# Optimization experiments

Hardware: AMD Instinct MI355X
Metric: run time of the kernel (lower is better)

The kernel has to match this reference:

```python
import jax, jax.numpy as jnp
import numpy as np

N_HEADS = 16
HEAD_DIM = 64


def apply_rope(x, cos, sin):
    # x: [B, H, S, D]; cos/sin: [S, D//2]
    x_even = x[..., ::2]
    x_odd = x[..., 1::2]
    c = cos[None, None, :, :]
    s = sin[None, None, :, :]
    rot_even = x_even * c - x_odd * s
    rot_odd = x_even * s + x_odd * c
    return jnp.stack((rot_even, rot_odd), axis=-1).reshape(x.shape)


def setup_inputs() -> dict:
    key = jax.random.key(0)
    ks = jax.random.split(key, 7)
    B, S, D = 2, 2048, 1024
    x = jax.random.normal(ks[0], (B, S, D), dtype=jnp.float32)
    # realistic rope tables
    inv_freq = 1.0 / (10000.0 ** (np.arange(0, HEAD_DIM, 2, dtype=np.float32) / HEAD_DIM))
    t = np.arange(S, dtype=np.float32)
    freqs = np.outer(t, inv_freq)  # [S, HEAD_DIM//2]
    rope_cos = jnp.asarray(np.cos(freqs), dtype=jnp.float32)
    rope_sin = jnp.asarray(np.sin(freqs), dtype=jnp.float32)
    Wqkv = jax.random.normal(ks[1], (D, 3 * D), dtype=jnp.float32) * (D ** -0.5)
    bqkv = jax.random.normal(ks[2], (3 * D,), dtype=jnp.float32) * 0.02
    Wout = jax.random.normal(ks[3], (D, D), dtype=jnp.float32) * (D ** -0.5)
    bout = jax.random.normal(ks[4], (D,), dtype=jnp.float32) * 0.02
    return {"x": x, "rope_cos": rope_cos, "rope_sin": rope_sin,
            "Wqkv": Wqkv, "bqkv": bqkv, "Wout": Wout, "bout": bout}


def reference(x, rope_cos, rope_sin, Wqkv, bqkv, Wout, bout):
    B, S, D = x.shape
    H, Hd = N_HEADS, HEAD_DIM
    qkv = x @ Wqkv + bqkv                      # [B, S, 3D]
    qkv = qkv.reshape(B, S, 3, H, Hd).transpose(2, 0, 3, 1, 4)  # [3, B, H, S, Hd]
    q, k, v = qkv[0], qkv[1], qkv[2]
    q = apply_rope(q, rope_cos, rope_sin)
    k = apply_rope(k, rope_cos, rope_sin)
    scale = Hd ** -0.5
    scores = jnp.einsum('bhqd,bhkd->bhqk', q, k) * scale
    causal = jnp.tril(jnp.ones((S, S), dtype=bool))
    scores = jnp.where(causal[None, None], scores, jnp.finfo(scores.dtype).min)
    attn = jax.nn.softmax(scores, axis=-1)
    out = jnp.einsum('bhqk,bhkd->bhqd', attn, v)  # [B, H, S, Hd]
    out = out.transpose(0, 2, 1, 3).reshape(B, S, D)
    return out @ Wout + bout
```

## Files before the change

kernel.cpp:

```cpp
#include <hip/hip_runtime.h>
#include <hip/hip_bf16.h>

typedef unsigned short u16;
typedef __attribute__((ext_vector_type(4))) float f32x4;
typedef __attribute__((ext_vector_type(16))) float f32x16;
typedef __attribute__((ext_vector_type(8))) short short8;
typedef __attribute__((ext_vector_type(8))) unsigned short ushort8;

__device__ __forceinline__ u16 f2bf(float f) {
  union { float f; unsigned u; } v; v.f = f;
  unsigned r = v.u + 0x7fffu + ((v.u >> 16) & 1u);
  return (u16)(r >> 16);
}
__device__ __forceinline__ float b2f(u16 h) {
  union { unsigned u; float f; } v; v.u = ((unsigned)h) << 16;
  return v.f;
}
__device__ __forceinline__ f32x4 mfma16(short8 a, short8 b, f32x4 c) {
  return __builtin_amdgcn_mfma_f32_16x16x32_bf16(a, b, c, 0, 0, 0);
}
__device__ __forceinline__ f32x16 mfma32(short8 a, short8 b, f32x16 c) {
  return __builtin_amdgcn_mfma_f32_32x32x16_bf16(a, b, c, 0, 0, 0);
}
__device__ __forceinline__ unsigned cvtpk(float a, float b) {
  unsigned r;
  asm("v_cvt_pk_bf16_f32 %0, %1, %2" : "=v"(r) : "v"(a), "v"(b));
  return r;
}
__device__ __forceinline__ short8 pack4(unsigned w0, unsigned w1, unsigned w2, unsigned w3) {
  union { unsigned u[4]; short8 s; } t;
  t.u[0] = w0; t.u[1] = w1; t.u[2] = w2; t.u[3] = w3;
  return t.s;
}
__device__ __forceinline__ float exp2h(float x) { return __builtin_amdgcn_exp2f(x); }

__global__ __launch_bounds__(256) void cvt_f32_bf16_k(const float* __restrict__ in,
                                                      u16* __restrict__ out, int n8) {
  int t = blockIdx.x * 256 + threadIdx.x;
  if (t >= n8) return;
  const float4* p = (const float4*)(in + (size_t)t * 8);
  float4 a = p[0], b = p[1];
  ushort8 o;
  o[0] = f2bf(a.x); o[1] = f2bf(a.y); o[2] = f2bf(a.z); o[3] = f2bf(a.w);
  o[4] = f2bf(b.x); o[5] = f2bf(b.y); o[6] = f2bf(b.z); o[7] = f2bf(b.w);
  *(ushort8*)(out + (size_t)t * 8) = o;
}

__global__ __launch_bounds__(256) void transpose_f32_bf16_k(const float* __restrict__ in,
                                                            u16* __restrict__ out, int R, int C) {
  __shared__ float tile[32][33];
  int bc = blockIdx.x * 32, br = blockIdx.y * 32;
  int tx = threadIdx.x & 31, ty = threadIdx.x >> 5;
#pragma unroll
  for (int p = 0; p < 4; ++p)
    tile[ty + p * 8][tx] = in[(size_t)(br + ty + p * 8) * C + bc + tx];
  __syncthreads();
#pragma unroll
  for (int p = 0; p < 4; ++p)
    out[(size_t)(bc + ty + p * 8) * R + br + tx] = f2bf(tile[tx][ty + p * 8]);
}

template <int MODE>
__global__ __launch_bounds__(256) void gemm_bt_k(const u16* __restrict__ A,
                                                 const u16* __restrict__ Bt,
                                                 const float* __restrict__ bias,
                                                 const float* __restrict__ cosT,
                                                 const float* __restrict__ sinT,
                                                 void* __restrict__ Cout) {
  __shared__ __align__(16) u16 As[128 * 32];
  __shared__ __align__(16) u16 Bs[128 * 32];
  const int tid = threadIdx.x, lane = tid & 63, w = tid >> 6;
  const int wr = w >> 1, wc = w & 1, g = lane >> 4, c16 = lane & 15;
  const int rowBase = blockIdx.y * 128, colBase = blockIdx.x * 128;
  f32x4 acc[4][4] = {};
  const int e0 = (w * 2 + 0) * 512 + lane * 8;
  const int e1 = (w * 2 + 1) * 512 + lane * 8;
  const u16* Ag0 = A + (size_t)(rowBase + (e0 >> 5)) * 1024 + (e0 & 31);
  const u16* Ag1 = A + (size_t)(rowBase + (e1 >> 5)) * 1024 + (e1 & 31);
  const u16* Bg0 = Bt + (size_t)(colBase + (e0 >> 5)) * 1024 + (e0 & 31);
  const u16* Bg1 = Bt + (size_t)(colBase + (e1 >> 5)) * 1024 + (e1 & 31);
  u16* As0 = As + (w * 2 + 0) * 512;
  u16* As1 = As + (w * 2 + 1) * 512;
  u16* Bs0 = Bs + (w * 2 + 0) * 512;
  u16* Bs1 = Bs + (w * 2 + 1) * 512;
  for (int k0 = 0; k0 < 1024; k0 += 32) {
    __builtin_amdgcn_global_load_lds((const __attribute__((address_space(1))) void*)(Ag0 + k0),
                                     (__attribute__((address_space(3))) void*)As0, 16, 0, 0);
    __builtin_amdgcn_global_load_lds((const __attribute__((address_space(1))) void*)(Ag1 + k0),
                                     (__attribute__((address_space(3))) void*)As1, 16, 0, 0);
    __builtin_amdgcn_global_load_lds((const __attribute__((address_space(1))) void*)(Bg0 + k0),
                                     (__attribute__((address_space(3))) void*)Bs0, 16, 0, 0);
    __builtin_amdgcn_global_load_lds((const __attribute__((address_space(1))) void*)(Bg1 + k0),
                                     (__attribute__((address_space(3))) void*)Bs1, 16, 0, 0);
    asm volatile("s_waitcnt vmcnt(0)" ::: "memory");
    __syncthreads();
    short8 af[4], bfr[4];
#pragma unroll
    for (int t = 0; t < 4; ++t)
      af[t] = *(const short8*)(As + ((wr * 64 + t * 16 + c16) * 32 + g * 8));
#pragma unroll
    for (int t = 0; t < 4; ++t)
      bfr[t] = *(const short8*)(Bs + ((wc * 64 + t * 16 + c16) * 32 + g * 8));
#pragma unroll
    for (int i = 0; i < 4; ++i)
#pragma unroll
      for (int j = 0; j < 4; ++j) acc[i][j] = mfma16(af[i], bfr[j], acc[i][j]);
    __syncthreads();
  }
#pragma unroll
  for (int i = 0; i < 4; ++i) {
    int mbase = rowBase + wr * 64 + i * 16 + 4 * g;
#pragma unroll
    for (int j = 0; j < 4; ++j) {
      int n = colBase + wc * 64 + j * 16 + c16;
      float bv = bias[n];
#pragma unroll
      for (int r = 0; r < 4; ++r) {
        float v = acc[i][j][r] + bv;
        int m = mbase + r;
        if (MODE == 0) {
          int which = n >> 10, hh = (n >> 6) & 15, d = n & 63;
          int bb = m >> 11, s = m & 2047;
          float outv = v;
          if (which < 2) {
            float pv = __shfl_xor(v, 1);
            float cc = cosT[(size_t)s * 32 + (d >> 1)];
            float ss = sinT[(size_t)s * 32 + (d >> 1)];
            outv = (d & 1) ? (v * cc + pv * ss) : (v * cc - pv * ss);
            if (which == 0) outv *= 0.18033688f;
          }
          ((u16*)Cout)[((size_t)(((which * 2 + bb) * 16 + hh) * 2048 + s) << 6) + d] = f2bf(outv);
        } else {
          ((float*)Cout)[(size_t)m * 1024 + n] = v;
        }
      }
    }
  }
}

__global__ __launch_bounds__(256) void vtrans_k(const u16* __restrict__ V, u16* __restrict__ Vt) {
  __shared__ u16 t[64][72];
  const int bh = blockIdx.y, s0 = blockIdx.x * 64;
  const u16* src = V + ((size_t)bh << 17);
  u16* dst = Vt + ((size_t)bh << 17);
  const int r = threadIdx.x >> 2, c0 = (threadIdx.x & 3) * 16;
  *(short8*)&t[r][c0] = *(const short8*)(src + (size_t)(s0 + r) * 64 + c0);
  *(short8*)&t[r][c0 + 8] = *(const short8*)(src + (size_t)(s0 + r) * 64 + c0 + 8);
  __syncthreads();
  const int d = threadIdx.x >> 2, sc0 = (threadIdx.x & 3) * 16;
  ushort8 o0, o1;
#pragma unroll
  for (int e = 0; e < 8; ++e) { o0[e] = t[sc0 + e][d]; o1[e] = t[sc0 + 8 + e][d]; }
  *(ushort8*)(dst + (size_t)d * 2048 + s0 + sc0) = o0;
  *(ushort8*)(dst + (size_t)d * 2048 + s0 + sc0 + 8) = o1;
}

__global__ __launch_bounds__(256, 2) void attn7_k(const u16* __restrict__ Qm,
                                                  const u16* __restrict__ Km,
                                                  const u16* __restrict__ Vtm,
                                                  u16* __restrict__ Om) {
  __shared__ __align__(16) u16 KL[2][4096];
  __shared__ __align__(16) u16 VL[2][4096];

  const int tid = threadIdx.x;
  const int lane = tid & 63, w = tid >> 6;
  const int x = blockIdx.x & 7;
  const int i = blockIdx.x >> 3;
  const int bh = 4 * x + (i & 3);
  const int rank = i >> 2;
  const int qm = (rank < 8) ? (15 - rank) : (rank - 8);
  const int b = bh >> 4, hd = bh & 15;
  const int qb = qm * 128 + w * 32;
  const int q32 = lane & 31, hl = lane >> 5;
  const int nt = 2 * qm + 2;

  const u16* Qp = Qm + ((size_t)bh << 17);
  const u16* Kp = Km + ((size_t)bh << 17);
  const u16* Vtp = Vtm + ((size_t)bh << 17);

  const u16* qrow = Qp + ((size_t)(qb + q32) << 6) + 8 * hl;
  short8 qf[4];
#pragma unroll
  for (int ks = 0; ks < 4; ++ks) qf[ks] = *(const short8*)(qrow + 16 * ks);

  f32x16 acc0 = {}, acc1 = {};
  float m_run = -1e30f, l_run = 0.f;
  const int qg = qb + q32;
  const int rr = w * 8 + (lane >> 3);
  const int sb = (lane & 7) ^ (lane >> 3);
  const int swz = q32 & 7;

  auto stage = [&](int buf, int k0s) {
    u16* kb = &KL[buf][w * 512];
    u16* vb = &VL[buf][w * 512];
    __builtin_amdgcn_global_load_lds(
        (const __attribute__((address_space(1))) void*)(Kp + ((size_t)(k0s + rr) << 6) + sb * 8),
        (__attribute__((address_space(3))) void*)kb, 16, 0, 0);
    __builtin_amdgcn_global_load_lds(
        (const __attribute__((address_space(1))) void*)(Kp + ((size_t)(k0s + rr + 32) << 6) + sb * 8),
        (__attribute__((address_space(3))) void*)(kb + 2048), 16, 0, 0);
    __builtin_amdgcn_global_load_lds(
        (const __attribute__((address_space(1))) void*)(Vtp + ((size_t)rr << 11) + k0s + sb * 8),
        (__attribute__((address_space(3))) void*)vb, 16, 0, 0);
    __builtin_amdgcn_global_load_lds(
        (const __attribute__((address_space(1))) void*)(Vtp + ((size_t)(rr + 32) << 11) + k0s + sb * 8),
        (__attribute__((address_space(3))) void*)(vb + 2048), 16, 0, 0);
  };

  stage(0, 0);
  asm volatile("s_waitcnt vmcnt(0)" ::: "memory");
  __syncthreads();

  for (int it = 0; it < nt; ++it) {
    const int cur = it & 1;
    if (it + 1 < nt) stage(cur ^ 1, 64 * (it + 1));
    const int k0 = 64 * it;

    if (k0 <= qb + 31) {
      const u16* Kb = &KL[cur][0];
      const u16* Vb = &VL[cur][0];

      f32x16 s0 = {}, s1 = {};
      __builtin_amdgcn_s_setprio(1);
#pragma unroll
      for (int ks = 0; ks < 4; ++ks) {
        const int cb = ((2 * ks + hl) ^ swz) * 8;
        short8 kf0 = *(const short8*)(Kb + q32 * 64 + cb);
        short8 kf1 = *(const short8*)(Kb + (32 + q32) * 64 + cb);
        s0 = mfma32(kf0, qf[ks], s0);
        s1 = mfma32(kf1, qf[ks], s1);
      }
      __builtin_amdgcn_s_setprio(0);

      short8 vfa[4], vfb[4];
#pragma unroll
      for (int ks = 0; ks < 4; ++ks) {
        const int cb = ((2 * ks + hl) ^ swz) * 8;
        vfa[ks] = *(const short8*)(Vb + q32 * 64 + cb);
        vfb[ks] = *(const short8*)(Vb + (32 + q32) * 64 + cb);
      }

      if (k0 + 63 > qb) {
#pragma unroll
        for (int r = 0; r < 16; ++r) {
          const int kvl = k0 + (r & 3) + 8 * (r >> 2) + 4 * hl;
          s0[r] = (kvl <= qg) ? s0[r] : -1e30f;
          s1[r] = (kvl + 32 <= qg) ? s1[r] : -1e30f;
        }
      }

      float pmax = s0[0];
#pragma unroll
      for (int r = 1; r < 16; ++r) pmax = fmaxf(pmax, s0[r]);
#pragma unroll
      for (int r = 0; r < 16; ++r) pmax = fmaxf(pmax, s1[r]);
      pmax = fmaxf(pmax, __shfl_xor(pmax, 32));

      if (!__all(pmax <= m_run + 11.5f)) {
        const float mn = fmaxf(m_run, pmax);
        const float alpha = exp2h(m_run - mn);
        l_run *= alpha;
        m_run = mn;
#pragma unroll
        for (int r = 0; r < 16; ++r) {
          const int row = (r & 3) + 8 * (r >> 2) + 4 * hl;
          const float ar = __shfl(alpha, row);
          acc0[r] *= ar; acc1[r] *= ar;
        }
      }

      float rs = 0.f;
#pragma unroll
      for (int r = 0; r < 16; ++r) { s0[r] = exp2h(s0[r] - m_run); rs += s0[r]; }
#pragma unroll
      for (int r = 0; r < 16; ++r) { s1[r] = exp2h(s1[r] - m_run); rs += s1[r]; }
      rs += __shfl_xor(rs, 32);
      l_run += rs;

      short8 pa[4];
#pragma unroll
      for (int t = 0; t < 2; ++t) {
        float p0, p1, p2, p3, p4, p5, p6, p7, p8, p9, pa_, pb_, pc_, pd_, pe_, pf_;
        if (t == 0) {
          p0 = s0[0];  p1 = s0[1];  p2 = s0[2];  p3 = s0[3];
          p4 = s0[4];  p5 = s0[5];  p6 = s0[6];  p7 = s0[7];
          p8 = s0[8];  p9 = s0[9];  pa_ = s0[10]; pb_ = s0[11];
          pc_ = s0[12]; pd_ = s0[13]; pe_ = s0[14]; pf_ = s0[15];
        } else {
          p0 = s1[0];  p1 = s1[1];  p2 = s1[2];  p3 = s1[3];
          p4 = s1[4];  p5 = s1[5];  p6 = s1[6];  p7 = s1[7];
          p8 = s1[8];  p9 = s1[9];  pa_ = s1[10]; pb_ = s1[11];
          pc_ = s1[12]; pd_ = s1[13]; pe_ = s1[14]; pf_ = s1[15];
        }
        const unsigned a0 = cvtpk(p0, p1), a1 = cvtpk(p2, p3);
        const unsigned a2 = cvtpk(p4, p5), a3 = cvtpk(p6, p7);
        const unsigned b0 = cvtpk(p8, p9), b1 = cvtpk(pa_, pb_);
        const unsigned b2 = cvtpk(pc_, pd_), b3 = cvtpk(pe_, pf_);
        const unsigned r0 = __shfl_xor(hl ? a0 : a2, 32);
        const unsigned r1 = __shfl_xor(hl ? a1 : a3, 32);
        pa[2 * t] = hl ? pack4(r0, r1, a2, a3) : pack4(a0, a1, r0, r1);
        const unsigned r2 = __shfl_xor(hl ? b0 : b2, 32);
        const unsigned r3 = __shfl_xor(hl ? b1 : b3, 32);
        pa[2 * t + 1] = hl ? pack4(r2, r3, b2, b3) : pack4(b0, b1, r2, r3);
      }

      __builtin_amdgcn_s_setprio(1);
#pragma unroll
      for (int ks = 0; ks < 4; ++ks) {
        acc0 = mfma32(pa[ks], vfa[ks], acc0);
        acc1 = mfma32(pa[ks], vfb[ks], acc1);
      }
      __builtin_amdgcn_s_setprio(0);
    }

    asm volatile("s_waitcnt vmcnt(0)" ::: "memory");
    __syncthreads();
  }

#pragma unroll
  for (int r = 0; r < 16; ++r) {
    const int row = (r & 3) + 8 * (r >> 2) + 4 * hl;
    const float li = 1.0f / __shfl(l_run, row);
    const int q = qb + row;
    const size_t base = ((size_t)(b * 2048 + q) << 10) + hd * 64 + q32;
    Om[base] = f2bf(acc0[r] * li);
    Om[base + 32] = f2bf(acc1[r] * li);
  }
}

extern "C" void kernel_launch(void* const* d_in, const int* in_sizes, int n_in,
                              void* d_out, int out_size, void* d_ws, size_t ws_size,
                              hipStream_t stream) {
  const float* x        = (const float*)d_in[0];
  const float* rope_cos = (const float*)d_in[1];
  const float* rope_sin = (const float*)d_in[2];
  const float* Wqkv     = (const float*)d_in[3];
  const float* bqkv     = (const float*)d_in[4];
  const float* Wout     = (const float*)d_in[5];
  const float* bout     = (const float*)d_in[6];
  float* out = (float*)d_out;
  char* ws = (char*)d_ws;

  u16* Xb      = (u16*)(ws);
  u16* WqkvT   = (u16*)(ws + 8388608);
  u16* WoutT   = (u16*)(ws + 14680064);
  u16* QKV     = (u16*)(ws + 16777216);
  u16* AttnOut = (u16*)(ws + 41943040);
  u16* Vt      = (u16*)(ws + 50331648);

  cvt_f32_bf16_k<<<dim3(2048), dim3(256), 0, stream>>>(x, Xb, 524288);
  transpose_f32_bf16_k<<<dim3(96, 32), dim3(256), 0, stream>>>(Wqkv, WqkvT, 1024, 3072);
  transpose_f32_bf16_k<<<dim3(32, 32), dim3(256), 0, stream>>>(Wout, WoutT, 1024, 1024);

  gemm_bt_k<0><<<dim3(24, 32), dim3(256), 0, stream>>>(Xb, WqkvT, bqkv, rope_cos, rope_sin,
                                                       (void*)QKV);

  u16* Qw = QKV;
  u16* Kw = QKV + (size_t)4194304;
  u16* Vw = QKV + (size_t)8388608;
  vtrans_k<<<dim3(32, 32), dim3(256), 0, stream>>>(Vw, Vt);
  attn7_k<<<dim3(512), dim3(256), 0, stream>>>(Qw, Kw, Vt, AttnOut);

  gemm_bt_k<1><<<dim3(8, 32), dim3(256), 0, stream>>>(AttnOut, WoutT, bout, nullptr, nullptr, out);
}
```

Measured before the change: 138.2 us.

## Replace QKV projection GEMM with 256x256-tiled, double-buffered, swizzled-LDS kernel

The QKV projection moves from 128x128 tiles with a 32-wide K step and a full wait every iteration to a new 512-thread kernel. It uses 256x256 tiles, a 64-wide K step, double-buffered LDS staging and an XOR-swizzled LDS layout, and interleaves global-to-LDS prefetch with MFMA quarters using sched barriers and setprio. The aim is more data reuse per tile, overlap of memory loads with compute, and fewer LDS bank conflicts in the largest GEMM. In exchange it needs 128 KB of LDS per block and many accumulator registers. With only 192 blocks it may underfill the 256 CUs. The output GEMM is split into its own plain kernel with no functional change.

New measurement: 150.1 us. 1.09x slower.

```diff
diff --git a/kernel.cpp b/kernel.cpp
--- a/kernel.cpp
+++ b/kernel.cpp
@@ -7,6 +7,9 @@
 typedef __attribute__((ext_vector_type(8))) short short8;
 typedef __attribute__((ext_vector_type(8))) unsigned short ushort8;
 
+#define AS1 __attribute__((address_space(1)))
+#define AS3 __attribute__((address_space(3)))
+
 __device__ __forceinline__ u16 f2bf(float f) {
   union { float f; unsigned u; } v; v.f = f;
   unsigned r = v.u + 0x7fffu + ((v.u >> 16) & 1u);
@@ -33,6 +36,9 @@
   return t.s;
 }
 __device__ __forceinline__ float exp2h(float x) { return __builtin_amdgcn_exp2f(x); }
+
+#define SBAR() do { __builtin_amdgcn_sched_barrier(0); __builtin_amdgcn_s_barrier(); \
+                    __builtin_amdgcn_sched_barrier(0); } while (0)
 
 __global__ __launch_bounds__(256) void cvt_f32_bf16_k(const float* __restrict__ in,
                                                       u16* __restrict__ out, int n8) {
@@ -60,13 +66,126 @@
     out[(size_t)(bc + ty + p * 8) * R + br + tx] = f2bf(tile[tx][ty + p * 8]);
 }
 
-template <int MODE>
-__global__ __launch_bounds__(256) void gemm_bt_k(const u16* __restrict__ A,
-                                                 const u16* __restrict__ Bt,
-                                                 const float* __restrict__ bias,
-                                                 const float* __restrict__ cosT,
-                                                 const float* __restrict__ sinT,
-                                                 void* __restrict__ Cout) {
+__global__ __launch_bounds__(512, 2) void gemm8_k(const u16* __restrict__ A,
+                                                  const u16* __restrict__ Bt,
+                                                  const float* __restrict__ bias,
+                                                  const float* __restrict__ cosT,
+                                                  const float* __restrict__ sinT,
+                                                  u16* __restrict__ Cout) {
+  __shared__ __align__(16) u16 As[2][16384];
+  __shared__ __align__(16) u16 Bs[2][16384];
+
+  const int tid = threadIdx.x, lane = tid & 63, w = tid >> 6;
+  const int wm = w >> 2, wn = w & 3;
+  const int g = lane >> 4, c16 = lane & 15;
+  const int l8 = lane >> 3, l7 = lane & 7;
+  const int bm = (blockIdx.x & 15) << 8;
+  const int bn = (blockIdx.x >> 4) << 8;
+
+  const int sw = (l7 ^ l8) * 8;
+  const int bs2 = (wn & 1) * 2 + wm;
+  const u16* Asrc = A + (size_t)(bm + wm * 128 + wn * 32 + l8) * 1024 + sw;
+  const u16* Bsrc = Bt + (size_t)(bn + (wn >> 1) * 128 + bs2 * 32 + l8) * 1024 + sw;
+  const int adst = wm * 8192 + wn * 2048;
+  const int bdst = (wn >> 1) * 8192 + bs2 * 2048;
+
+  f32x4 acc[8][4] = {};
+  short8 afr[8], bfr[8];
+  const int swr = (c16 & 7);
+
+#define STAGE_A(buf, kt) do { _Pragma("unroll") for (int j = 0; j < 4; ++j) \
+    __builtin_amdgcn_global_load_lds((const AS1 void*)(Asrc + (size_t)j * 8192 + (kt) * 64), \
+                                     (AS3 void*)(&As[buf][adst + j * 512]), 16, 0, 0); } while (0)
+#define STAGE_B(buf, kt) do { _Pragma("unroll") for (int j = 0; j < 4; ++j) \
+    __builtin_amdgcn_global_load_lds((const AS1 void*)(Bsrc + (size_t)j * 8192 + (kt) * 64), \
+                                     (AS3 void*)(&Bs[buf][bdst + j * 512]), 16, 0, 0); } while (0)
+#define LD_A(cur, MB) do { _Pragma("unroll") for (int mi = 0; mi < 4; ++mi) \
+    _Pragma("unroll") for (int kc = 0; kc < 2; ++kc) \
+      afr[mi * 2 + kc] = *(const short8*)(&As[cur][wm * 8192 + (((MB) + mi) * 16 + c16) * 64 + \
+                                                   (((kc * 4 + g) ^ swr) * 8)]); } while (0)
+#define LD_B(cur, NB, OFS) do { _Pragma("unroll") for (int nj = 0; nj < 2; ++nj) \
+    _Pragma("unroll") for (int kc = 0; kc < 2; ++kc) \
+      bfr[(OFS) + nj * 2 + kc] = *(const short8*)(&Bs[cur][(wn >> 1) * 8192 + \
+          ((wn & 1) * 64 + ((NB) + nj) * 16 + c16) * 64 + (((kc * 4 + g) ^ swr) * 8)]); } while (0)
+#define MFMA_Q(MB, NB, BOFS) do { _Pragma("unroll") for (int mi = 0; mi < 4; ++mi) \
+    _Pragma("unroll") for (int nj = 0; nj < 2; ++nj) \
+    _Pragma("unroll") for (int kc = 0; kc < 2; ++kc) \
+      acc[(MB) + mi][(NB) + nj] = mfma16(afr[mi * 2 + kc], bfr[(BOFS) + nj * 2 + kc], \
+                                         acc[(MB) + mi][(NB) + nj]); } while (0)
+
+  STAGE_A(0, 0);
+  STAGE_B(0, 0);
+  asm volatile("s_waitcnt vmcnt(0)" ::: "memory");
+  SBAR();
+
+  for (int t = 0; t < 16; ++t) {
+    const int cur = t & 1;
+    const bool pre = (t + 1 < 16);
+    LD_A(cur, 0);
+    LD_B(cur, 0, 0);
+    if (pre) STAGE_A(cur ^ 1, t + 1);
+    SBAR();
+    __builtin_amdgcn_s_setprio(1);
+    MFMA_Q(0, 0, 0);
+    __builtin_amdgcn_s_setprio(0);
+    SBAR();
+    LD_B(cur, 2, 4);
+    if (pre) STAGE_B(cur ^ 1, t + 1);
+    SBAR();
+    __builtin_amdgcn_s_setprio(1);
+    MFMA_Q(0, 2, 4);
+    __builtin_amdgcn_s_setprio(0);
+    SBAR();
+    LD_A(cur, 4);
+    SBAR();
+    __builtin_amdgcn_s_setprio(1);
+    MFMA_Q(4, 0, 0);
+    __builtin_amdgcn_s_setprio(0);
+    SBAR();
+    if (pre) { asm volatile("s_waitcnt vmcnt(0)" ::: "memory"); }
+    SBAR();
+    __builtin_amdgcn_s_setprio(1);
+    MFMA_Q(4, 2, 4);
+    __builtin_amdgcn_s_setprio(0);
+    SBAR();
+  }
+
+#pragma unroll
+  for (int mi = 0; mi < 8; ++mi) {
+    const int mbase = bm + wm * 128 + mi * 16 + 4 * g;
+#pragma unroll
+    for (int nj = 0; nj < 4; ++nj) {
+      const int n = bn + wn * 64 + nj * 16 + c16;
+      const float bv = bias[n];
+      const int which = n >> 10, hh = (n >> 6) & 15, d = n & 63;
+#pragma unroll
+      for (int r = 0; r < 4; ++r) {
+        float v = acc[mi][nj][r] + bv;
+        const int m = mbase + r;
+        const int bb = m >> 11, s = m & 2047;
+        float outv = v;
+        if (which < 2) {
+          float pv = __shfl_xor(v, 1);
+          float cc = cosT[(size_t)s * 32 + (d >> 1)];
+          float ssn = sinT[(size_t)s * 32 + (d >> 1)];
+          outv = (d & 1) ? (v * cc + pv * ssn) : (v * cc - pv * ssn);
+          if (which == 0) outv *= 0.18033688f;
+        }
+        Cout[((size_t)(((which * 2 + bb) * 16 + hh) * 2048 + s) << 6) + d] = f2bf(outv);
+      }
+    }
+  }
+#undef STAGE_A
+#undef STAGE_B
+#undef LD_A
+#undef LD_B
+#undef MFMA_Q
+}
+
+__global__ __launch_bounds__(256) void gemm_out_k(const u16* __restrict__ A,
+                                                  const u16* __restrict__ Bt,
+                                                  const float* __restrict__ bias,
+                                                  float* __restrict__ Cout) {
   __shared__ __align__(16) u16 As[128 * 32];
   __shared__ __align__(16) u16 Bs[128 * 32];
   const int tid = threadIdx.x, lane = tid & 63, w = tid >> 6;
@@ -84,27 +203,23 @@
   u16* Bs0 = Bs + (w * 2 + 0) * 512;
   u16* Bs1 = Bs + (w * 2 + 1) * 512;
   for (int k0 = 0; k0 < 1024; k0 += 32) {
-    __builtin_amdgcn_global_load_lds((const __attribute__((address_space(1))) void*)(Ag0 + k0),
-                                     (__attribute__((address_space(3))) void*)As0, 16, 0, 0);
-    __builtin_amdgcn_global_load_lds((const __attribute__((address_space(1))) void*)(Ag1 + k0),
-                                     (__attribute__((address_space(3))) void*)As1, 16, 0, 0);
-    __builtin_amdgcn_global_load_lds((const __attribute__((address_space(1))) void*)(Bg0 + k0),
-                                     (__attribute__((address_space(3))) void*)Bs0, 16, 0, 0);
-    __builtin_amdgcn_global_load_lds((const __attribute__((address_space(1))) void*)(Bg1 + k0),
-                                     (__attribute__((address_space(3))) void*)Bs1, 16, 0, 0);
+    __builtin_amdgcn_global_load_lds((const AS1 void*)(Ag0 + k0), (AS3 void*)As0, 16, 0, 0);
+    __builtin_amdgcn_global_load_lds((const AS1 void*)(Ag1 + k0), (AS3 void*)As1, 16, 0, 0);
+    __builtin_amdgcn_global_load_lds((const AS1 void*)(Bg0 + k0), (AS3 void*)Bs0, 16, 0, 0);
+    __builtin_amdgcn_global_load_lds((const AS1 void*)(Bg1 + k0), (AS3 void*)Bs1, 16, 0, 0);
     asm volatile("s_waitcnt vmcnt(0)" ::: "memory");
     __syncthreads();
-    short8 af[4], bfr[4];
+    short8 af[4], bfr2[4];
 #pragma unroll
     for (int t = 0; t < 4; ++t)
       af[t] = *(const short8*)(As + ((wr * 64 + t * 16 + c16) * 32 + g * 8));
 #pragma unroll
     for (int t = 0; t < 4; ++t)
-      bfr[t] = *(const short8*)(Bs + ((wc * 64 + t * 16 + c16) * 32 + g * 8));
+      bfr2[t] = *(const short8*)(Bs + ((wc * 64 + t * 16 + c16) * 32 + g * 8));
 #pragma unroll
     for (int i = 0; i < 4; ++i)
 #pragma unroll
-      for (int j = 0; j < 4; ++j) acc[i][j] = mfma16(af[i], bfr[j], acc[i][j]);
+      for (int j = 0; j < 4; ++j) acc[i][j] = mfma16(af[i], bfr2[j], acc[i][j]);
     __syncthreads();
   }
 #pragma unroll
@@ -115,25 +230,8 @@
       int n = colBase + wc * 64 + j * 16 + c16;
       float bv = bias[n];
 #pragma unroll
-      for (int r = 0; r < 4; ++r) {
-        float v = acc[i][j][r] + bv;
-        int m = mbase + r;
-        if (MODE == 0) {
-          int which = n >> 10, hh = (n >> 6) & 15, d = n & 63;
-          int bb = m >> 11, s = m & 2047;
-          float outv = v;
-          if (which < 2) {
-            float pv = __shfl_xor(v, 1);
-            float cc = cosT[(size_t)s * 32 + (d >> 1)];
-            float ss = sinT[(size_t)s * 32 + (d >> 1)];
-            outv = (d & 1) ? (v * cc + pv * ss) : (v * cc - pv * ss);
-            if (which == 0) outv *= 0.18033688f;
-          }
-          ((u16*)Cout)[((size_t)(((which * 2 + bb) * 16 + hh) * 2048 + s) << 6) + d] = f2bf(outv);
-        } else {
-          ((float*)Cout)[(size_t)m * 1024 + n] = v;
-        }
-      }
+      for (int r = 0; r < 4; ++r)
+        Cout[(size_t)(mbase + r) * 1024 + n] = acc[i][j][r] + bv;
     }
   }
 }
@@ -194,17 +292,17 @@
     u16* kb = &KL[buf][w * 512];
     u16* vb = &VL[buf][w * 512];
     __builtin_amdgcn_global_load_lds(
-        (const __attribute__((address_space(1))) void*)(Kp + ((size_t)(k0s + rr) << 6) + sb * 8),
-        (__attribute__((address_space(3))) void*)kb, 16, 0, 0);
+        (const AS1 void*)(Kp + ((size_t)(k0s + rr) << 6) + sb * 8),
+        (AS3 void*)kb, 16, 0, 0);
     __builtin_amdgcn_global_load_lds(
-        (const __attribute__((address_space(1))) void*)(Kp + ((size_t)(k0s + rr + 32) << 6) + sb * 8),
-        (__attribute__((address_space(3))) void*)(kb + 2048), 16, 0, 0);
+        (const AS1 void*)(Kp + ((size_t)(k0s + rr + 32) << 6) + sb * 8),
+        (AS3 void*)(kb + 2048), 16, 0, 0);
     __builtin_amdgcn_global_load_lds(
-        (const __attribute__((address_space(1))) void*)(Vtp + ((size_t)rr << 11) + k0s + sb * 8),
-        (__attribute__((address_space(3))) void*)vb, 16, 0, 0);
+        (const AS1 void*)(Vtp + ((size_t)rr << 11) + k0s + sb * 8),
+        (AS3 void*)vb, 16, 0, 0);
     __builtin_amdgcn_global_load_lds(
-        (const __attribute__((address_space(1))) void*)(Vtp + ((size_t)(rr + 32) << 11) + k0s + sb * 8),
-        (__attribute__((address_space(3))) void*)(vb + 2048), 16, 0, 0);
+        (const AS1 void*)(Vtp + ((size_t)(rr + 32) << 11) + k0s + sb * 8),
+        (AS3 void*)(vb + 2048), 16, 0, 0);
   };
 
   stage(0, 0);
@@ -352,8 +450,7 @@
   transpose_f32_bf16_k<<<dim3(96, 32), dim3(256), 0, stream>>>(Wqkv, WqkvT, 1024, 3072);
   transpose_f32_bf16_k<<<dim3(32, 32), dim3(256), 0, stream>>>(Wout, WoutT, 1024, 1024);
 
-  gemm_bt_k<0><<<dim3(24, 32), dim3(256), 0, stream>>>(Xb, WqkvT, bqkv, rope_cos, rope_sin,
-                                                       (void*)QKV);
+  gemm8_k<<<dim3(192), dim3(512), 0, stream>>>(Xb, WqkvT, bqkv, rope_cos, rope_sin, QKV);
 
   u16* Qw = QKV;
   u16* Kw = QKV + (size_t)4194304;
@@ -361,5 +458,5 @@
   vtrans_k<<<dim3(32, 32), dim3(256), 0, stream>>>(Vw, Vt);
   attn7_k<<<dim3(512), dim3(256), 0, stream>>>(Qw, Kw, Vt, AttnOut);
 
-  gemm_bt_k<1><<<dim3(8, 32), dim3(256), 0, stream>>>(AttnOut, WoutT, bout, nullptr, nullptr, out);
-}
+  gemm_out_k<<<dim3(8, 32), dim3(256), 0, stream>>>(AttnOut, WoutT, bout, out);
+}
```

## Split attention into 64-query blocks of two waves with snake-order scheduling

Applied to the files above, without the earlier changes.

The attention kernel now uses 128-thread blocks, each covering 64 query rows, and launches twice as many blocks. The causal tile count per block becomes qm+1, so no fully-masked KV tile is ever visited, and the per-tile skip branch is removed. Query blocks are assigned in a serpentine order within groups of eight to balance work across the grid. In exchange, each K/V tile staged into LDS is shared by only two waves instead of four, so global-to-LDS traffic per unit of compute goes up.

Result: slower. 145.0 us (+4.9%).

```diff
diff --git a/kernel.cpp b/kernel.cpp
--- a/kernel.cpp
+++ b/kernel.cpp
@@ -6,6 +6,9 @@
 typedef __attribute__((ext_vector_type(16))) float f32x16;
 typedef __attribute__((ext_vector_type(8))) short short8;
 typedef __attribute__((ext_vector_type(8))) unsigned short ushort8;
+
+#define AS1 __attribute__((address_space(1)))
+#define AS3 __attribute__((address_space(3)))
 
 __device__ __forceinline__ u16 f2bf(float f) {
   union { float f; unsigned u; } v; v.f = f;
@@ -84,14 +87,10 @@
   u16* Bs0 = Bs + (w * 2 + 0) * 512;
   u16* Bs1 = Bs + (w * 2 + 1) * 512;
   for (int k0 = 0; k0 < 1024; k0 += 32) {
-    __builtin_amdgcn_global_load_lds((const __attribute__((address_space(1))) void*)(Ag0 + k0),
-                                     (__attribute__((address_space(3))) void*)As0, 16, 0, 0);
-    __builtin_amdgcn_global_load_lds((const __attribute__((address_space(1))) void*)(Ag1 + k0),
-                                     (__attribute__((address_space(3))) void*)As1, 16, 0, 0);
-    __builtin_amdgcn_global_load_lds((const __attribute__((address_space(1))) void*)(Bg0 + k0),
-                                     (__attribute__((address_space(3))) void*)Bs0, 16, 0, 0);
-    __builtin_amdgcn_global_load_lds((const __attribute__((address_space(1))) void*)(Bg1 + k0),
-                                     (__attribute__((address_space(3))) void*)Bs1, 16, 0, 0);
+    __builtin_amdgcn_global_load_lds((const AS1 void*)(Ag0 + k0), (AS3 void*)As0, 16, 0, 0);
+    __builtin_amdgcn_global_load_lds((const AS1 void*)(Ag1 + k0), (AS3 void*)As1, 16, 0, 0);
+    __builtin_amdgcn_global_load_lds((const AS1 void*)(Bg0 + k0), (AS3 void*)Bs0, 16, 0, 0);
+    __builtin_amdgcn_global_load_lds((const AS1 void*)(Bg1 + k0), (AS3 void*)Bs1, 16, 0, 0);
     asm volatile("s_waitcnt vmcnt(0)" ::: "memory");
     __syncthreads();
     short8 af[4], bfr[4];
@@ -155,7 +154,7 @@
   *(ushort8*)(dst + (size_t)d * 2048 + s0 + sc0 + 8) = o1;
 }
 
-__global__ __launch_bounds__(256, 2) void attn7_k(const u16* __restrict__ Qm,
+__global__ __launch_bounds__(128, 4) void attn8_k(const u16* __restrict__ Qm,
                                                   const u16* __restrict__ Km,
                                                   const u16* __restrict__ Vtm,
                                                   u16* __restrict__ Om) {
@@ -168,11 +167,12 @@
   const int i = blockIdx.x >> 3;
   const int bh = 4 * x + (i & 3);
   const int rank = i >> 2;
-  const int qm = (rank < 8) ? (15 - rank) : (rank - 8);
+  const int sl = rank >> 3, g8 = rank & 7;
+  const int qm = (sl & 1) ? (8 * sl + 7 - g8) : (8 * sl + g8);
   const int b = bh >> 4, hd = bh & 15;
-  const int qb = qm * 128 + w * 32;
+  const int qb = qm * 64 + w * 32;
   const int q32 = lane & 31, hl = lane >> 5;
-  const int nt = 2 * qm + 2;
+  const int nt = qm + 1;
 
   const u16* Qp = Qm + ((size_t)bh << 17);
   const u16* Kp = Km + ((size_t)bh << 17);
@@ -186,25 +186,23 @@
   f32x16 acc0 = {}, acc1 = {};
   float m_run = -1e30f, l_run = 0.f;
   const int qg = qb + q32;
-  const int rr = w * 8 + (lane >> 3);
-  const int sb = (lane & 7) ^ (lane >> 3);
+  const int r8 = lane >> 3;
+  const int sb = (lane & 7) ^ r8;
   const int swz = q32 & 7;
 
   auto stage = [&](int buf, int k0s) {
-    u16* kb = &KL[buf][w * 512];
-    u16* vb = &VL[buf][w * 512];
-    __builtin_amdgcn_global_load_lds(
-        (const __attribute__((address_space(1))) void*)(Kp + ((size_t)(k0s + rr) << 6) + sb * 8),
-        (__attribute__((address_space(3))) void*)kb, 16, 0, 0);
-    __builtin_amdgcn_global_load_lds(
-        (const __attribute__((address_space(1))) void*)(Kp + ((size_t)(k0s + rr + 32) << 6) + sb * 8),
-        (__attribute__((address_space(3))) void*)(kb + 2048), 16, 0, 0);
-    __builtin_amdgcn_global_load_lds(
-        (const __attribute__((address_space(1))) void*)(Vtp + ((size_t)rr << 11) + k0s + sb * 8),
-        (__attribute__((address_space(3))) void*)vb, 16, 0, 0);
-    __builtin_amdgcn_global_load_lds(
-        (const __attribute__((address_space(1))) void*)(Vtp + ((size_t)(rr + 32) << 11) + k0s + sb * 8),
-        (__attribute__((address_space(3))) void*)(vb + 2048), 16, 0, 0);
+#pragma unroll
+    for (int j = 0; j < 4; ++j) {
+      const int row = j * 16 + w * 8 + r8;
+      const u16* ksrc = Kp + ((size_t)(k0s + row) << 6) + sb * 8;
+      __builtin_amdgcn_global_load_lds(
+          (const AS1 void*)ksrc,
+          (AS3 void*)(&KL[buf][(j * 16 + w * 8) * 64]), 16, 0, 0);
+      const u16* vsrc = Vtp + ((size_t)row << 11) + k0s + sb * 8;
+      __builtin_amdgcn_global_load_lds(
+          (const AS1 void*)vsrc,
+          (AS3 void*)(&VL[buf][(j * 16 + w * 8) * 64]), 16, 0, 0);
+    }
   };
 
   stage(0, 0);
@@ -216,102 +214,100 @@
     if (it + 1 < nt) stage(cur ^ 1, 64 * (it + 1));
     const int k0 = 64 * it;
 
-    if (k0 <= qb + 31) {
-      const u16* Kb = &KL[cur][0];
-      const u16* Vb = &VL[cur][0];
-
-      f32x16 s0 = {}, s1 = {};
-      __builtin_amdgcn_s_setprio(1);
-#pragma unroll
-      for (int ks = 0; ks < 4; ++ks) {
-        const int cb = ((2 * ks + hl) ^ swz) * 8;
-        short8 kf0 = *(const short8*)(Kb + q32 * 64 + cb);
-        short8 kf1 = *(const short8*)(Kb + (32 + q32) * 64 + cb);
-        s0 = mfma32(kf0, qf[ks], s0);
-        s1 = mfma32(kf1, qf[ks], s1);
+    const u16* Kb = &KL[cur][0];
+    const u16* Vb = &VL[cur][0];
+
+    f32x16 s0 = {}, s1 = {};
+    __builtin_amdgcn_s_setprio(1);
+#pragma unroll
+    for (int ks = 0; ks < 4; ++ks) {
+      const int cb = ((2 * ks + hl) ^ swz) * 8;
+      short8 kf0 = *(const short8*)(Kb + q32 * 64 + cb);
+      short8 kf1 = *(const short8*)(Kb + (32 + q32) * 64 + cb);
+      s0 = mfma32(kf0, qf[ks], s0);
+      s1 = mfma32(kf1, qf[ks], s1);
+    }
+    __builtin_amdgcn_s_setprio(0);
+
+    short8 vfa[4], vfb[4];
+#pragma unroll
+    for (int ks = 0; ks < 4; ++ks) {
+      const int cb = ((2 * ks + hl) ^ swz) * 8;
+      vfa[ks] = *(const short8*)(Vb + q32 * 64 + cb);
+      vfb[ks] = *(const short8*)(Vb + (32 + q32) * 64 + cb);
+    }
+
+    if (k0 + 63 > qb) {
+#pragma unroll
+      for (int r = 0; r < 16; ++r) {
+        const int kvl = k0 + (r & 3) + 8 * (r >> 2) + 4 * hl;
+        s0[r] = (kvl <= qg) ? s0[r] : -1e30f;
+        s1[r] = (kvl + 32 <= qg) ? s1[r] : -1e30f;
       }
-      __builtin_amdgcn_s_setprio(0);
-
-      short8 vfa[4], vfb[4];
-#pragma unroll
-      for (int ks = 0; ks < 4; ++ks) {
-        const int cb = ((2 * ks + hl) ^ swz) * 8;
-        vfa[ks] = *(const short8*)(Vb + q32 * 64 + cb);
-        vfb[ks] = *(const short8*)(Vb + (32 + q32) * 64 + cb);
+    }
+
+    float pmax = s0[0];
+#pragma unroll
+    for (int r = 1; r < 16; ++r) pmax = fmaxf(pmax, s0[r]);
+#pragma unroll
+    for (int r = 0; r < 16; ++r) pmax = fmaxf(pmax, s1[r]);
+    pmax = fmaxf(pmax, __shfl_xor(pmax, 32));
+
+    if (!__all(pmax <= m_run + 11.5f)) {
+      const float mn = fmaxf(m_run, pmax);
+      const float alpha = exp2h(m_run - mn);
+      l_run *= alpha;
+      m_run = mn;
+#pragma unroll
+      for (int r = 0; r < 16; ++r) {
+        const int row = (r & 3) + 8 * (r >> 2) + 4 * hl;
+        const float ar = __shfl(alpha, row);
+        acc0[r] *= ar; acc1[r] *= ar;
       }
-
-      if (k0 + 63 > qb) {
-#pragma unroll
-        for (int r = 0; r < 16; ++r) {
-          const int kvl = k0 + (r & 3) + 8 * (r >> 2) + 4 * hl;
-          s0[r] = (kvl <= qg) ? s0[r] : -1e30f;
-          s1[r] = (kvl + 32 <= qg) ? s1[r] : -1e30f;
-        }
+    }
+
+    float rs = 0.f;
+#pragma unroll
+    for (int r = 0; r < 16; ++r) { s0[r] = exp2h(s0[r] - m_run); rs += s0[r]; }
+#pragma unroll
+    for (int r = 0; r < 16; ++r) { s1[r] = exp2h(s1[r] - m_run); rs += s1[r]; }
+    rs += __shfl_xor(rs, 32);
+    l_run += rs;
+
+    short8 pa[4];
+#pragma unroll
+    for (int t = 0; t < 2; ++t) {
+      float p0, p1, p2, p3, p4, p5, p6, p7, p8, p9, pa_, pb_, pc_, pd_, pe_, pf_;
+      if (t == 0) {
+        p0 = s0[0];  p1 = s0[1];  p2 = s0[2];  p3 = s0[3];
+        p4 = s0[4];  p5 = s0[5];  p6 = s0[6];  p7 = s0[7];
+        p8 = s0[8];  p9 = s0[9];  pa_ = s0[10]; pb_ = s0[11];
+        pc_ = s0[12]; pd_ = s0[13]; pe_ = s0[14]; pf_ = s0[15];
+      } else {
+        p0 = s1[0];  p1 = s1[1];  p2 = s1[2];  p3 = s1[3];
+        p4 = s1[4];  p5 = s1[5];  p6 = s1[6];  p7 = s1[7];
+        p8 = s1[8];  p9 = s1[9];  pa_ = s1[10]; pb_ = s1[11];
+        pc_ = s1[12]; pd_ = s1[13]; pe_ = s1[14]; pf_ = s1[15];
       }
-
-      float pmax = s0[0];
-#pragma unroll
-      for (int r = 1; r < 16; ++r) pmax = fmaxf(pmax, s0[r]);
-#pragma unroll
-      for (int r = 0; r < 16; ++r) pmax = fmaxf(pmax, s1[r]);
-      pmax = fmaxf(pmax, __shfl_xor(pmax, 32));
-
-      if (!__all(pmax <= m_run + 11.5f)) {
-        const float mn = fmaxf(m_run, pmax);
-        const float alpha = exp2h(m_run - mn);
-        l_run *= alpha;
-        m_run = mn;
-#pragma unroll
-        for (int r = 0; r < 16; ++r) {
-          const int row = (r & 3) + 8 * (r >> 2) + 4 * hl;
-          const float ar = __shfl(alpha, row);
-          acc0[r] *= ar; acc1[r] *= ar;
-        }
-      }
-
-      float rs = 0.f;
-#pragma unroll
-      for (int r = 0; r < 16; ++r) { s0[r] = exp2h(s0[r] - m_run); rs += s0[r]; }
-#pragma unroll
-      for (int r = 0; r < 16; ++r) { s1[r] = exp2h(s1[r] - m_run); rs += s1[r]; }
-      rs += __shfl_xor(rs, 32);
-      l_run += rs;
-
-      short8 pa[4];
-#pragma unroll
-      for (int t = 0; t < 2; ++t) {
-        float p0, p1, p2, p3, p4, p5, p6, p7, p8, p9, pa_, pb_, pc_, pd_, pe_, pf_;
-        if (t == 0) {
-          p0 = s0[0];  p1 = s0[1];  p2 = s0[2];  p3 = s0[3];
-          p4 = s0[4];  p5 = s0[5];  p6 = s0[6];  p7 = s0[7];
-          p8 = s0[8];  p9 = s0[9];  pa_ = s0[10]; pb_ = s0[11];
-          pc_ = s0[12]; pd_ = s0[13]; pe_ = s0[14]; pf_ = s0[15];
-        } else {
-          p0 = s1[0];  p1 = s1[1];  p2 = s1[2];  p3 = s1[3];
-          p4 = s1[4];  p5 = s1[5];  p6 = s1[6];  p7 = s1[7];
-          p8 = s1[8];  p9 = s1[9];  pa_ = s1[10]; pb_ = s1[11];
-          pc_ = s1[12]; pd_ = s1[13]; pe_ = s1[14]; pf_ = s1[15];
-        }
-        const unsigned a0 = cvtpk(p0, p1), a1 = cvtpk(p2, p3);
-        const unsigned a2 = cvtpk(p4, p5), a3 = cvtpk(p6, p7);
-        const unsigned b0 = cvtpk(p8, p9), b1 = cvtpk(pa_, pb_);
-        const unsigned b2 = cvtpk(pc_, pd_), b3 = cvtpk(pe_, pf_);
-        const unsigned r0 = __shfl_xor(hl ? a0 : a2, 32);
-        const unsigned r1 = __shfl_xor(hl ? a1 : a3, 32);
-        pa[2 * t] = hl ? pack4(r0, r1, a2, a3) : pack4(a0, a1, r0, r1);
-        const unsigned r2 = __shfl_xor(hl ? b0 : b2, 32);
-        const unsigned r3 = __shfl_xor(hl ? b1 : b3, 32);
-        pa[2 * t + 1] = hl ? pack4(r2, r3, b2, b3) : pack4(b0, b1, r2, r3);
-      }
-
-      __builtin_amdgcn_s_setprio(1);
-#pragma unroll
-      for (int ks = 0; ks < 4; ++ks) {
-        acc0 = mfma32(pa[ks], vfa[ks], acc0);
-        acc1 = mfma32(pa[ks], vfb[ks], acc1);
-      }
-      __builtin_amdgcn_s_setprio(0);
-    }
+      const unsigned a0 = cvtpk(p0, p1), a1 = cvtpk(p2, p3);
+      const unsigned a2 = cvtpk(p4, p5), a3 = cvtpk(p6, p7);
+      const unsigned b0 = cvtpk(p8, p9), b1 = cvtpk(pa_, pb_);
+      const unsigned b2 = cvtpk(pc_, pd_), b3 = cvtpk(pe_, pf_);
+      const unsigned r0 = __shfl_xor(hl ? a0 : a2, 32);
+      const unsigned r1 = __shfl_xor(hl ? a1 : a3, 32);
+      pa[2 * t] = hl ? pack4(r0, r1, a2, a3) : pack4(a0, a1, r0, r1);
+      const unsigned r2 = __shfl_xor(hl ? b0 : b2, 32);
+      const unsigned r3 = __shfl_xor(hl ? b1 : b3, 32);
+      pa[2 * t + 1] = hl ? pack4(r2, r3, b2, b3) : pack4(b0, b1, r2, r3);
+    }
+
+    __builtin_amdgcn_s_setprio(1);
+#pragma unroll
+    for (int ks = 0; ks < 4; ++ks) {
+      acc0 = mfma32(pa[ks], vfa[ks], acc0);
+      acc1 = mfma32(pa[ks], vfb[ks], acc1);
+    }
+    __builtin_amdgcn_s_setprio(0);
 
     asm volatile("s_waitcnt vmcnt(0)" ::: "memory");
     __syncthreads();
@@ -359,7 +355,7 @@
   u16* Kw = QKV + (size_t)4194304;
   u16* Vw = QKV + (size_t)8388608;
   vtrans_k<<<dim3(32, 32), dim3(256), 0, stream>>>(Vw, Vt);
-  attn7_k<<<dim3(512), dim3(256), 0, stream>>>(Qw, Kw, Vt, AttnOut);
+  attn8_k<<<dim3(1024), dim3(128), 0, stream>>>(Qw, Kw, Vt, AttnOut);
 
   gemm_bt_k<1><<<dim3(8, 32), dim3(256), 0, stream>>>(AttnOut, WoutT, bout, nullptr, nullptr, out);
 }
```

## Double GEMM K-tile to 64 with XOR-swizzled LDS layout

Applied to the files above, without the earlier changes.

The projection GEMM now stages a 64-wide K slice per iteration instead of 32, halving the number of barrier/wait rounds over K. The LDS tile rows are 64 elements with an XOR swizzle on 16-byte chunks, applied on the global-load side and matched on the fragment reads, to avoid bank conflicts. LDS use doubles and each wave issues twice the MMAs per sync. The attention kernel is only touched cosmetically with address-space macros.

After: 156.3 us. 13.1% more time.

```diff
diff --git a/kernel.cpp b/kernel.cpp
--- a/kernel.cpp
+++ b/kernel.cpp
@@ -6,6 +6,9 @@
 typedef __attribute__((ext_vector_type(16))) float f32x16;
 typedef __attribute__((ext_vector_type(8))) short short8;
 typedef __attribute__((ext_vector_type(8))) unsigned short ushort8;
+
+#define AS1 __attribute__((address_space(1)))
+#define AS3 __attribute__((address_space(3)))
 
 __device__ __forceinline__ u16 f2bf(float f) {
   union { float f; unsigned u; } v; v.f = f;
@@ -67,46 +70,55 @@
                                                  const float* __restrict__ cosT,
                                                  const float* __restrict__ sinT,
                                                  void* __restrict__ Cout) {
-  __shared__ __align__(16) u16 As[128 * 32];
-  __shared__ __align__(16) u16 Bs[128 * 32];
+  __shared__ __align__(16) u16 As[128 * 64];
+  __shared__ __align__(16) u16 Bs[128 * 64];
   const int tid = threadIdx.x, lane = tid & 63, w = tid >> 6;
   const int wr = w >> 1, wc = w & 1, g = lane >> 4, c16 = lane & 15;
   const int rowBase = blockIdx.y * 128, colBase = blockIdx.x * 128;
+  const int r8 = lane >> 3, l7 = lane & 7;
+  const int sb = l7 ^ r8;
   f32x4 acc[4][4] = {};
-  const int e0 = (w * 2 + 0) * 512 + lane * 8;
-  const int e1 = (w * 2 + 1) * 512 + lane * 8;
-  const u16* Ag0 = A + (size_t)(rowBase + (e0 >> 5)) * 1024 + (e0 & 31);
-  const u16* Ag1 = A + (size_t)(rowBase + (e1 >> 5)) * 1024 + (e1 & 31);
-  const u16* Bg0 = Bt + (size_t)(colBase + (e0 >> 5)) * 1024 + (e0 & 31);
-  const u16* Bg1 = Bt + (size_t)(colBase + (e1 >> 5)) * 1024 + (e1 & 31);
-  u16* As0 = As + (w * 2 + 0) * 512;
-  u16* As1 = As + (w * 2 + 1) * 512;
-  u16* Bs0 = Bs + (w * 2 + 0) * 512;
-  u16* Bs1 = Bs + (w * 2 + 1) * 512;
-  for (int k0 = 0; k0 < 1024; k0 += 32) {
-    __builtin_amdgcn_global_load_lds((const __attribute__((address_space(1))) void*)(Ag0 + k0),
-                                     (__attribute__((address_space(3))) void*)As0, 16, 0, 0);
-    __builtin_amdgcn_global_load_lds((const __attribute__((address_space(1))) void*)(Ag1 + k0),
-                                     (__attribute__((address_space(3))) void*)As1, 16, 0, 0);
-    __builtin_amdgcn_global_load_lds((const __attribute__((address_space(1))) void*)(Bg0 + k0),
-                                     (__attribute__((address_space(3))) void*)Bs0, 16, 0, 0);
-    __builtin_amdgcn_global_load_lds((const __attribute__((address_space(1))) void*)(Bg1 + k0),
-                                     (__attribute__((address_space(3))) void*)Bs1, 16, 0, 0);
+
+  const u16* Ag[4];
+  const u16* Bg[4];
+#pragma unroll
+  for (int j = 0; j < 4; ++j) {
+    const int row = w * 32 + j * 8 + r8;
+    Ag[j] = A + (size_t)(rowBase + row) * 1024 + sb * 8;
+    Bg[j] = Bt + (size_t)(colBase + row) * 1024 + sb * 8;
+  }
+
+  for (int k0 = 0; k0 < 1024; k0 += 64) {
+#pragma unroll
+    for (int j = 0; j < 4; ++j) {
+      __builtin_amdgcn_global_load_lds((const AS1 void*)(Ag[j] + k0),
+                                       (AS3 void*)(As + (w * 2048 + j * 512)), 16, 0, 0);
+      __builtin_amdgcn_global_load_lds((const AS1 void*)(Bg[j] + k0),
+                                       (AS3 void*)(Bs + (w * 2048 + j * 512)), 16, 0, 0);
+    }
     asm volatile("s_waitcnt vmcnt(0)" ::: "memory");
     __syncthreads();
-    short8 af[4], bfr[4];
+    const int swr = c16 & 7;
+    short8 af[4][2], bfr[4][2];
 #pragma unroll
     for (int t = 0; t < 4; ++t)
-      af[t] = *(const short8*)(As + ((wr * 64 + t * 16 + c16) * 32 + g * 8));
-#pragma unroll
-    for (int t = 0; t < 4; ++t)
-      bfr[t] = *(const short8*)(Bs + ((wc * 64 + t * 16 + c16) * 32 + g * 8));
+#pragma unroll
+      for (int kc = 0; kc < 2; ++kc) {
+        af[t][kc] = *(const short8*)(As + (wr * 64 + t * 16 + c16) * 64 +
+                                     (((kc * 4 + g) ^ swr) * 8));
+        bfr[t][kc] = *(const short8*)(Bs + (wc * 64 + t * 16 + c16) * 64 +
+                                      (((kc * 4 + g) ^ swr) * 8));
+      }
 #pragma unroll
     for (int i = 0; i < 4; ++i)
 #pragma unroll
-      for (int j = 0; j < 4; ++j) acc[i][j] = mfma16(af[i], bfr[j], acc[i][j]);
+      for (int j = 0; j < 4; ++j) {
+        acc[i][j] = mfma16(af[i][0], bfr[j][0], acc[i][j]);
+        acc[i][j] = mfma16(af[i][1], bfr[j][1], acc[i][j]);
+      }
     __syncthreads();
   }
+
 #pragma unroll
   for (int i = 0; i < 4; ++i) {
     int mbase = rowBase + wr * 64 + i * 16 + 4 * g;
@@ -194,17 +206,17 @@
     u16* kb = &KL[buf][w * 512];
     u16* vb = &VL[buf][w * 512];
     __builtin_amdgcn_global_load_lds(
-        (const __attribute__((address_space(1))) void*)(Kp + ((size_t)(k0s + rr) << 6) + sb * 8),
-        (__attribute__((address_space(3))) void*)kb, 16, 0, 0);
+        (const AS1 void*)(Kp + ((size_t)(k0s + rr) << 6) + sb * 8),
+        (AS3 void*)kb, 16, 0, 0);
     __builtin_amdgcn_global_load_lds(
-        (const __attribute__((address_space(1))) void*)(Kp + ((size_t)(k0s + rr + 32) << 6) + sb * 8),
-        (__attribute__((address_space(3))) void*)(kb + 2048), 16, 0, 0);
+        (const AS1 void*)(Kp + ((size_t)(k0s + rr + 32) << 6) + sb * 8),
+        (AS3 void*)(kb + 2048), 16, 0, 0);
     __builtin_amdgcn_global_load_lds(
-        (const __attribute__((address_space(1))) void*)(Vtp + ((size_t)rr << 11) + k0s + sb * 8),
-        (__attribute__((address_space(3))) void*)vb, 16, 0, 0);
+        (const AS1 void*)(Vtp + ((size_t)rr << 11) + k0s + sb * 8),
+        (AS3 void*)vb, 16, 0, 0);
     __builtin_amdgcn_global_load_lds(
-        (const __attribute__((address_space(1))) void*)(Vtp + ((size_t)(rr + 32) << 11) + k0s + sb * 8),
-        (__attribute__((address_space(3))) void*)(vb + 2048), 16, 0, 0);
+        (const AS1 void*)(Vtp + ((size_t)(rr + 32) << 11) + k0s + sb * 8),
+        (AS3 void*)(vb + 2048), 16, 0, 0);
   };
 
   stage(0, 0);
```
